# Kernel optimization log

Hardware: AMD Instinct MI355X
Metric: run time of the kernel (lower is better)

## Reference

```python
import jax, jax.numpy as jnp
import numpy as np

BLOCK = (4, 8, 8)   # (t, h, w)
NH, D, DA = 8, 512, 64
EPS = 1e-5


def _layernorm(x, g, b):
    m = jnp.mean(x, axis=-1, keepdims=True)
    xc = x - m
    v = jnp.mean(xc * xc, axis=-1, keepdims=True)
    return xc * jax.lax.rsqrt(v + EPS) * g + b


def setup_inputs() -> dict:
    key = jax.random.key(0)
    ks = jax.random.split(key, 10)
    B, T, H, W = 2, 8, 32, 32
    t, h, w = BLOCK
    s_qkv = (2.0 / (D + DA)) ** 0.5   # xavier_normal for (d, da) fan
    s_lin = (2.0 / (D + D)) ** 0.5
    return {
        "x": jax.random.normal(ks[0], (B, D, T, H, W), jnp.float32),
        "dt_bank": 0.02 * jax.random.normal(ks[1], (NH, 2 * t - 1), jnp.float32),
        "dh_bank": 0.02 * jax.random.normal(ks[2], (NH, 2 * h - 1), jnp.float32),
        "dw_bank": 0.02 * jax.random.normal(ks[3], (NH, 2 * w - 1), jnp.float32),
        "ln1_g": jnp.ones((D,), jnp.float32),
        "ln1_b": jnp.zeros((D,), jnp.float32),
        "w_q": s_qkv * jax.random.normal(ks[4], (NH, D, DA), jnp.float32),
        "w_k": s_qkv * jax.random.normal(ks[5], (NH, D, DA), jnp.float32),
        "w_v": s_qkv * jax.random.normal(ks[6], (NH, D, DA), jnp.float32),
        "w_proj": s_lin * jax.random.normal(ks[7], (D, NH * DA), jnp.float32),
        "ln2_g": jnp.ones((D,), jnp.float32),
        "ln2_b": jnp.zeros((D,), jnp.float32),
        "w1": s_lin * jax.random.normal(ks[8], (D, D), jnp.float32),
        "b1": jnp.zeros((D,), jnp.float32),
        "w2": s_lin * jax.random.normal(ks[9], (D, D), jnp.float32),
        "b2": jnp.zeros((D,), jnp.float32),
    }


def _axial_bias(dt_bank, dh_bank, dw_bank):
    t, h, w = BLOCK
    thw = t * h * w
    ar = jnp.arange(thw)
    tt = ar // (h * w)
    hh = (ar // w) % h
    ww = ar % w
    # relative offsets shifted to be non-negative (matches dt += abs(dt.min()))
    it = tt[:, None] - tt[None, :] + (t - 1)
    ih = hh[:, None] - hh[None, :] + (h - 1)
    iw = ww[:, None] - ww[None, :] + (w - 1)
    return dt_bank[:, it] + dh_bank[:, ih] + dw_bank[:, iw]  # (NH, thw, thw)


def reference(x, dt_bank, dh_bank, dw_bank, ln1_g, ln1_b, w_q, w_k, w_v,
              w_proj, ln2_g, ln2_b, w1, b1, w2, b2):
    B, C, T, H, W = x.shape
    t, h, w = BLOCK
    st, sh, sw = T // t, H // h, W // w
    thw = t * h * w
    nb = B * st * sh * sw

    # block split: (B,C,T,H,W) -> (nb, thw, C)
    xb = x.reshape(B, C, st, t, sh, h, sw, w).transpose(0, 2, 4, 6, 1, 3, 5, 7)
    xb = xb.reshape(nb, C, thw).transpose(0, 2, 1)

    Bb = _axial_bias(dt_bank, dh_bank, dw_bank)  # (NH, thw, thw)

    # --- multi-head attention with additive axial bias ---
    resid = xb
    xn = _layernorm(xb, ln1_g, ln1_b)
    q = jnp.einsum('bnd,hde->hbne', xn, w_q)
    k = jnp.einsum('bnd,hde->hbne', xn, w_k)
    v = jnp.einsum('bnd,hde->hbne', xn, w_v)
    scale = 1.0 / jnp.sqrt(jnp.asarray(DA, x.dtype))
    attn = jnp.einsum('hbne,hbme->hbnm', q, k) * scale + Bb[:, None]
    attn = jax.nn.softmax(attn, axis=-1)
    out = jnp.einsum('hbnm,hbme->hbne', attn, v)         # (NH, nb, thw, DA)
    out = out.transpose(1, 2, 0, 3).reshape(nb, thw, NH * DA)  # head-major concat
    out = out @ w_proj.T + resid

    # --- FFN with residual ---
    y = _layernorm(out, ln2_g, ln2_b)
    y = jax.nn.relu(y @ w1.T + b1) @ w2.T + b2
    out = y + out

    # un-block: (nb, thw, C) -> (B,C,T,H,W)
    out = out.transpose(0, 2, 1).reshape(B, st, sh, sw, C, t, h, w)
    out = out.transpose(0, 4, 1, 5, 2, 6, 3, 7).reshape(B, C, T, H, W)
    return out
```

## Files before the change

kernel.cpp:

```cpp
#include <hip/hip_runtime.h>
#include <hip/hip_bf16.h>
#include <stdint.h>

typedef __attribute__((ext_vector_type(4))) float f32x4;
typedef __attribute__((ext_vector_type(8))) short s16x8;
typedef __attribute__((ext_vector_type(4))) short s16x4;
typedef __attribute__((ext_vector_type(8))) __bf16 b16x8;

__device__ __forceinline__ f32x4 mfma16(s16x8 a, s16x8 b, f32x4 c) {
  return __builtin_amdgcn_mfma_f32_16x16x32_bf16(
      __builtin_bit_cast(b16x8, a), __builtin_bit_cast(b16x8, b), c, 0, 0, 0);
}

__device__ __forceinline__ void gl_lds16(const void* g, void* l) {
  __builtin_amdgcn_global_load_lds(
      (const __attribute__((address_space(1))) void*)g,
      (__attribute__((address_space(3))) void*)l, 16, 0, 0);
}

__device__ __forceinline__ unsigned short f2bf(float f) {
  union { float f; unsigned u; } v; v.f = f;
  unsigned u = v.u;
  return (unsigned short)((u + 0x7FFFu + ((u >> 16) & 1u)) >> 16);
}

__device__ __forceinline__ float bf2f(unsigned short u) {
  union { unsigned u; float f; } v; v.u = ((unsigned)u) << 16; return v.f;
}

__device__ __forceinline__ unsigned cvt_pk_bf16(float a, float b) {
  unsigned r;
  asm("v_cvt_pk_bf16_f32 %0, %1, %2" : "=v"(r) : "v"(a), "v"(b));
  return r;
}

#if __has_builtin(__builtin_amdgcn_exp2f)
#define EXP2F(x) __builtin_amdgcn_exp2f(x)
#else
#define EXP2F(x) exp2f(x)
#endif

__global__ __launch_bounds__(256) void k_gather_ln(
    const float* __restrict__ x, const float* __restrict__ g1, const float* __restrict__ b1,
    unsigned short* __restrict__ xb, unsigned short* __restrict__ xn,
    const float* __restrict__ wq, const float* __restrict__ wk, const float* __restrict__ wv,
    const float* __restrict__ wp, const float* __restrict__ w1, const float* __restrict__ w2,
    unsigned short* __restrict__ qkvT, unsigned short* __restrict__ wpT,
    unsigned short* __restrict__ w1T, unsigned short* __restrict__ w2T)
{
  if (blockIdx.x >= 1024) {
    int i = (blockIdx.x - 1024) * 256 + threadIdx.x;
    if (i < 786432) {
      int n = i >> 9, d = i & 511;
      const float* src = (n < 512) ? wq : (n < 1024 ? wk : wv);
      int nn = n & 511;
      int h = nn >> 6, e = nn & 63;
      qkvT[i] = f2bf(src[((size_t)h * 512 + d) * 64 + e]);
    } else {
      int j = i - 786432;
      int w = j >> 18;
      int o = j & 262143;
      const float* s = (w == 0) ? wp : (w == 1 ? w1 : w2);
      unsigned short* dst = (w == 0) ? wpT : (w == 1 ? w1T : w2T);
      dst[o] = f2bf(s[o]);
    }
    return;
  }
  __shared__ float lx[16][517];
  int gid = blockIdx.x;
  int h2 = gid & 1, hh = (gid >> 1) & 7, tt = (gid >> 4) & 3,
      shI = (gid >> 6) & 3, stI = (gid >> 8) & 1, bI = (gid >> 9) & 1;
  const float* xbase = x + (size_t)bI * 4194304 + (size_t)(stI * 4 + tt) * 1024
                       + (shI * 8 + hh) * 32 + h2 * 16;
  int t = threadIdx.x;
  for (int i = 0; i < 8; ++i) {
    int slot = i * 256 + t;
    int c = slot >> 2, w8 = slot & 3;
    const float4 v = *(const float4*)(xbase + (size_t)c * 8192 + w8 * 4);
    lx[w8 * 4 + 0][c] = v.x; lx[w8 * 4 + 1][c] = v.y;
    lx[w8 * 4 + 2][c] = v.z; lx[w8 * 4 + 3][c] = v.w;
  }
  __syncthreads();
  int lane = t & 63, wid = t >> 6;
  for (int q = 0; q < 4; ++q) {
    int widx = wid * 4 + q;
    float vv[8]; float s = 0.f, ss = 0.f;
    #pragma unroll
    for (int i = 0; i < 8; ++i) { float v = lx[widx][lane + i * 64]; vv[i] = v; s += v; ss += v * v; }
    #pragma unroll
    for (int d = 1; d < 64; d <<= 1) { s += __shfl_xor(s, d); ss += __shfl_xor(ss, d); }
    float mean = s * (1.f / 512.f);
    float var = ss * (1.f / 512.f) - mean * mean;
    float rs = rsqrtf(var + 1e-5f);
    int sw = h2 * 2 + (widx >> 3), ww = widx & 7;
    int blk = ((bI * 2 + stI) * 4 + shI) * 4 + sw;
    int n = tt * 64 + hh * 8 + ww;
    size_t base = ((size_t)blk * 256 + n) * 512;
    #pragma unroll
    for (int i = 0; i < 8; ++i) {
      int c = lane + i * 64;
      float v = vv[i];
      xb[base + c] = f2bf(v);
      xn[base + c] = f2bf((v - mean) * rs * g1[c] + b1[c]);
    }
  }
}

template<int EPI>
__global__ __launch_bounds__(256, 2) void k_gemm(
    const unsigned short* __restrict__ A, const unsigned short* __restrict__ Bt,
    int M, int N,
    unsigned short* __restrict__ Cbf, float* __restrict__ Cf,
    const float* __restrict__ bias,
    const unsigned short* __restrict__ addbf,
    unsigned short* __restrict__ vTout)
{
  constexpr int K = 512;
  __shared__ __align__(16) unsigned short a_lds[2][128 * 64];
  __shared__ __align__(16) unsigned short b_lds[2][128 * 64];
  int tid = threadIdx.x, lane = tid & 63, wid = tid >> 6;
  int lin = blockIdx.y * gridDim.x + blockIdx.x;
  int xcd = lin & 7, idx = lin >> 3;
  int bx = xcd * 16 + (idx & 15);
  int by = idx >> 4;
  int m0 = bx * 128, n0 = by * 128;
  int wm = (wid >> 1) * 64, wn = (wid & 1) * 64;
  int r15 = lane & 15, g = lane >> 4;

  const unsigned short* aptr[4];
  const unsigned short* bptr[4];
  int segoff[4];
  #pragma unroll
  for (int s = 0; s < 4; ++s) {
    int seg = wid * 4 + s;
    int slot = seg * 64 + lane;
    int m = slot >> 3, lc = (slot & 7) ^ (m & 7);
    aptr[s] = A + (size_t)(m0 + m) * K + lc * 8;
    bptr[s] = Bt + (size_t)(n0 + m) * K + lc * 8;
    segoff[s] = seg * 1024;
  }

  f32x4 acc[4][4] = {};

  #pragma unroll
  for (int s = 0; s < 4; ++s) {
    gl_lds16(aptr[s], (char*)a_lds[0] + segoff[s]);
    gl_lds16(bptr[s], (char*)b_lds[0] + segoff[s]);
  }

  #pragma unroll
  for (int it = 0; it < 8; ++it) {
    int cur = it & 1;
    if (it < 7) {
      int ksn = (it + 1) * 64;
      #pragma unroll
      for (int s = 0; s < 4; ++s) {
        gl_lds16(aptr[s] + ksn, (char*)a_lds[cur ^ 1] + segoff[s]);
        gl_lds16(bptr[s] + ksn, (char*)b_lds[cur ^ 1] + segoff[s]);
      }
      asm volatile("s_waitcnt vmcnt(8)" ::: "memory");
    } else {
      asm volatile("s_waitcnt vmcnt(0)" ::: "memory");
    }
    __builtin_amdgcn_s_barrier();
    __builtin_amdgcn_sched_barrier(0);
    const char* al = (const char*)a_lds[cur];
    const char* bl = (const char*)b_lds[cur];
    #pragma unroll
    for (int kk = 0; kk < 2; ++kk) {
      s16x8 af[4], bfr[4];
      #pragma unroll
      for (int f = 0; f < 4; ++f) {
        int mm = wm + f * 16 + r15;
        af[f] = *(const s16x8*)(al + mm * 128 + (((kk * 4 + g) ^ (mm & 7)) * 16));
        int nn = wn + f * 16 + r15;
        bfr[f] = *(const s16x8*)(bl + nn * 128 + (((kk * 4 + g) ^ (nn & 7)) * 16));
      }
      __builtin_amdgcn_s_setprio(1);
      #pragma unroll
      for (int fm = 0; fm < 4; ++fm)
        #pragma unroll
        for (int fn = 0; fn < 4; ++fn)
          acc[fm][fn] = mfma16(af[fm], bfr[fn], acc[fm][fn]);
      __builtin_amdgcn_s_setprio(0);
    }
    __builtin_amdgcn_s_barrier();
    __builtin_amdgcn_sched_barrier(0);
  }

  int g4 = g * 4;
  #pragma unroll
  for (int fm = 0; fm < 4; ++fm) {
    #pragma unroll
    for (int fn = 0; fn < 4; ++fn) {
      int col = n0 + wn + fn * 16 + r15;
      int row0 = m0 + wm + fm * 16 + g4;
      if (EPI == 0 && col >= 1024) {
        int h = (col - 1024) >> 6, e = col & 63;
        int blk = row0 >> 8, mtok = row0 & 255;
        s16x4 pk;
        #pragma unroll
        for (int r = 0; r < 4; ++r) pk[r] = (short)f2bf(acc[fm][fn][r]);
        *(s16x4*)(vTout + (((size_t)blk * 8 + h) * 64 + e) * 256 + mtok) = pk;
      } else {
        #pragma unroll
        for (int r = 0; r < 4; ++r) {
          int row = row0 + r;
          float v = acc[fm][fn][r];
          if (EPI == 0) {
            Cbf[(size_t)row * 1536 + col] = f2bf(v);
          } else if (EPI == 1) {
            Cbf[(size_t)row * 512 + col] = f2bf(v + bf2f(addbf[(size_t)row * 512 + col]));
          } else if (EPI == 2) {
            Cbf[(size_t)row * 512 + col] = f2bf(fmaxf(v + bias[col], 0.f));
          } else {
            Cf[(size_t)row * 512 + col] = v + bias[col] + bf2f(addbf[(size_t)row * 512 + col]);
          }
        }
      }
    }
  }
}

__global__ __launch_bounds__(256, 1) void k_attn(
    const unsigned short* __restrict__ qkv, const unsigned short* __restrict__ vT,
    const float* __restrict__ dtb, const float* __restrict__ dhb, const float* __restrict__ dwb,
    unsigned short* __restrict__ aout)
{
  __shared__ __align__(16) unsigned short k_lds[2][64 * 64];
  __shared__ __align__(16) unsigned short v_lds[2][64 * 64];
  __shared__ __align__(16) unsigned short p_lds[4][64 * 64];
  __shared__ float bt_s[8], bh_s[16], bw_s[16];

  const float L2E = 1.44269504f;
  const float SC = 0.125f * 1.44269504f;

  int tid = threadIdx.x, lane = tid & 63, wid = tid >> 6;
  int bk = blockIdx.x >> 3, h = blockIdx.x & 7;
  if (tid < 7) bt_s[tid] = dtb[h * 7 + tid] * L2E;
  else if (tid < 22) bh_s[tid - 7] = dhb[h * 15 + tid - 7] * L2E;
  else if (tid < 37) bw_s[tid - 22] = dwb[h * 15 + tid - 22] * L2E;

  int r15 = lane & 15, g = lane >> 4;
  int wq0 = wid * 64;
  size_t bkBase = (size_t)bk * 256;
  const unsigned short* kbase = qkv + 512 + h * 64;
  const unsigned short* vbase = vT + ((size_t)bk * 8 + h) * 64 * 256;

  s16x8 qf[4][2];
  #pragma unroll
  for (int fn = 0; fn < 4; ++fn)
    #pragma unroll
    for (int kk = 0; kk < 2; ++kk)
      qf[fn][kk] = *(const s16x8*)(qkv + (bkBase + wq0 + fn * 16 + r15) * 1536
                                   + h * 64 + kk * 32 + g * 8);

  float btoff[4], hb[7], wb[4];

  #pragma unroll
  for (int s = 0; s < 4; ++s) {
    int sg = wid * 4 + s;
    if (sg < 8) {
      int slot = sg * 64 + lane;
      int m = slot >> 3, lc = (slot & 7) ^ (m & 7);
      gl_lds16(kbase + (bkBase + m) * 1536 + lc * 8, (char*)(&k_lds[0][0]) + sg * 1024);
    } else {
      int sg2 = sg - 8;
      int slot = sg2 * 64 + lane;
      int e = slot >> 3, lc = (slot & 7) ^ (e & 7);
      gl_lds16(vbase + (size_t)e * 256 + lc * 8, (char*)(&v_lds[0][0]) + sg2 * 1024);
    }
  }
  __syncthreads();

  {
    int Dh = (r15 >> 3) - (g >> 1) + 7;
    int Wb = (r15 & 7) - 4 * (g & 1) + 7;
    #pragma unroll
    for (int mt = 0; mt < 4; ++mt) btoff[mt] = bt_s[wid + 3 - mt];
    #pragma unroll
    for (int d = 0; d < 7; ++d) hb[d] = bh_s[Dh + 2 * d - 6];
    #pragma unroll
    for (int r = 0; r < 4; ++r) wb[r] = bw_s[Wb - r];
  }

  f32x4 o[4][4] = {};
  float mrun[4] = {-1e30f, -1e30f, -1e30f, -1e30f};
  float lrun[4] = {0.f, 0.f, 0.f, 0.f};
  char* p_w = (char*)(&p_lds[wid][0]);

  #pragma unroll
  for (int mt = 0; mt < 4; ++mt) {
    int cur = mt & 1;
    if (mt < 3) {
      int m0n = (mt + 1) * 64;
      #pragma unroll
      for (int s = 0; s < 4; ++s) {
        int sg = wid * 4 + s;
        if (sg < 8) {
          int slot = sg * 64 + lane;
          int m = slot >> 3, lc = (slot & 7) ^ (m & 7);
          gl_lds16(kbase + (bkBase + m0n + m) * 1536 + lc * 8,
                   (char*)(&k_lds[cur ^ 1][0]) + sg * 1024);
        } else {
          int sg2 = sg - 8;
          int slot = sg2 * 64 + lane;
          int e = slot >> 3, lc = (slot & 7) ^ (e & 7);
          gl_lds16(vbase + (size_t)e * 256 + m0n + lc * 8,
                   (char*)(&v_lds[cur ^ 1][0]) + sg2 * 1024);
        }
      }
    }
    if (mt > 0) {
      if (mt < 3) asm volatile("s_waitcnt vmcnt(4)" ::: "memory");
      else        asm volatile("s_waitcnt vmcnt(0)" ::: "memory");
      __builtin_amdgcn_s_barrier();
      __builtin_amdgcn_sched_barrier(0);
    }
    const char* kl = (const char*)(&k_lds[cur][0]);
    const char* vl = (const char*)(&v_lds[cur][0]);

    f32x4 st[4][4] = {};
    #pragma unroll
    for (int kk = 0; kk < 2; ++kk) {
      s16x8 kf[4];
      #pragma unroll
      for (int fm = 0; fm < 4; ++fm) {
        int m = fm * 16 + r15;
        kf[fm] = *(const s16x8*)(kl + m * 128 + (((kk * 4 + g) ^ (m & 7)) * 16));
      }
      __builtin_amdgcn_s_setprio(1);
      #pragma unroll
      for (int fm = 0; fm < 4; ++fm)
        #pragma unroll
        for (int fn = 0; fn < 4; ++fn)
          st[fm][fn] = mfma16(kf[fm], qf[fn][kk], st[fm][fn]);
      __builtin_amdgcn_s_setprio(0);
    }

    #pragma unroll
    for (int fn = 0; fn < 4; ++fn) {
      float vals[16];
      float mx = -1e30f;
      #pragma unroll
      for (int fm = 0; fm < 4; ++fm) {
        float cc = btoff[mt] + hb[fn - fm + 3];
        #pragma unroll
        for (int r = 0; r < 4; ++r) {
          float v = fmaf(st[fm][fn][r], SC, cc) + wb[r];
          vals[fm * 4 + r] = v;
          mx = fmaxf(mx, v);
        }
      }
      mx = fmaxf(mx, __shfl_xor(mx, 16));
      mx = fmaxf(mx, __shfl_xor(mx, 32));
      if (!__all(mx <= mrun[fn] + 8.f)) {
        float mnew = fmaxf(mrun[fn], mx);
        float al = EXP2F(mrun[fn] - mnew);
        mrun[fn] = mnew;
        lrun[fn] *= al;
        #pragma unroll
        for (int fe = 0; fe < 4; ++fe)
          #pragma unroll
          for (int r = 0; r < 4; ++r)
            o[fe][fn][r] *= al;
      }
      float m_c = mrun[fn];
      float p[16]; float sum = 0.f;
      #pragma unroll
      for (int i = 0; i < 16; ++i) { p[i] = EXP2F(vals[i] - m_c); sum += p[i]; }
      sum += __shfl_xor(sum, 16);
      sum += __shfl_xor(sum, 32);
      lrun[fn] += sum;
      int nl = fn * 16 + r15;
      char* prow = p_w + nl * 128 + (g & 1) * 8;
      #pragma unroll
      for (int fm = 0; fm < 4; ++fm) {
        unsigned u0 = cvt_pk_bf16(p[fm * 4 + 0], p[fm * 4 + 1]);
        unsigned u1 = cvt_pk_bf16(p[fm * 4 + 2], p[fm * 4 + 3]);
        int lc = fm * 2 + (g >> 1);
        *(uint2*)(prow + ((lc ^ (nl & 7)) * 16)) = make_uint2(u0, u1);
      }
    }
    asm volatile("s_waitcnt lgkmcnt(0)" ::: "memory");
    __builtin_amdgcn_sched_barrier(0);

    #pragma unroll
    for (int mm = 0; mm < 2; ++mm) {
      s16x8 vf[4], pf[4];
      #pragma unroll
      for (int fe = 0; fe < 4; ++fe) {
        int e = fe * 16 + r15;
        vf[fe] = *(const s16x8*)(vl + e * 128 + (((mm * 4 + g) ^ (e & 7)) * 16));
      }
      #pragma unroll
      for (int fn = 0; fn < 4; ++fn) {
        int nl = fn * 16 + r15;
        pf[fn] = *(const s16x8*)(p_w + nl * 128 + (((mm * 4 + g) ^ (nl & 7)) * 16));
      }
      __builtin_amdgcn_s_setprio(1);
      #pragma unroll
      for (int fe = 0; fe < 4; ++fe)
        #pragma unroll
        for (int fn = 0; fn < 4; ++fn)
          o[fe][fn] = mfma16(vf[fe], pf[fn], o[fe][fn]);
      __builtin_amdgcn_s_setprio(0);
    }
    __builtin_amdgcn_s_barrier();
    __builtin_amdgcn_sched_barrier(0);
  }

  #pragma unroll
  for (int fn = 0; fn < 4; ++fn) {
    float inv = 1.f / lrun[fn];
    size_t rowb = (bkBase + wq0 + fn * 16 + r15) * 512 + h * 64;
    #pragma unroll
    for (int fe = 0; fe < 4; ++fe) {
      unsigned u0 = cvt_pk_bf16(o[fe][fn][0] * inv, o[fe][fn][1] * inv);
      unsigned u1 = cvt_pk_bf16(o[fe][fn][2] * inv, o[fe][fn][3] * inv);
      *(uint2*)(aout + rowb + fe * 16 + g * 4) = make_uint2(u0, u1);
    }
  }
}

__global__ __launch_bounds__(256) void k_ln2(
    const unsigned short* __restrict__ in, const float* __restrict__ g2, const float* __restrict__ b2,
    unsigned short* __restrict__ out)
{
  int token = blockIdx.x * 4 + (threadIdx.x >> 6);
  int lane = threadIdx.x & 63;
  s16x8 v8 = *(const s16x8*)(in + (size_t)token * 512 + lane * 8);
  float vv[8]; float s = 0.f, ss = 0.f;
  #pragma unroll
  for (int i = 0; i < 8; ++i) {
    float v = bf2f((unsigned short)v8[i]); vv[i] = v; s += v; ss += v * v;
  }
  #pragma unroll
  for (int d = 1; d < 64; d <<= 1) { s += __shfl_xor(s, d); ss += __shfl_xor(ss, d); }
  float mean = s * (1.f / 512.f);
  float var = ss * (1.f / 512.f) - mean * mean;
  float rs = rsqrtf(var + 1e-5f);
  const float4 gA = *(const float4*)(g2 + lane * 8);
  const float4 gB = *(const float4*)(g2 + lane * 8 + 4);
  const float4 bA = *(const float4*)(b2 + lane * 8);
  const float4 bB = *(const float4*)(b2 + lane * 8 + 4);
  float gv[8] = {gA.x, gA.y, gA.z, gA.w, gB.x, gB.y, gB.z, gB.w};
  float bv[8] = {bA.x, bA.y, bA.z, bA.w, bB.x, bB.y, bB.z, bB.w};
  s16x8 o8;
  #pragma unroll
  for (int i = 0; i < 8; ++i)
    o8[i] = (short)f2bf((vv[i] - mean) * rs * gv[i] + bv[i]);
  *(s16x8*)(out + (size_t)token * 512 + lane * 8) = o8;
}

__global__ __launch_bounds__(64) void k_scatter(
    const float* __restrict__ fin, float* __restrict__ out)
{
  __shared__ float lx[32][33];
  int gid = blockIdx.x;
  int cc = gid & 15;
  int sg = gid >> 4;
  int hh = sg & 7, tt = (sg >> 3) & 3, shI = (sg >> 5) & 3, stI = (sg >> 7) & 1, bI = (sg >> 8) & 1;
  int c0 = cc * 32;
  int l = threadIdx.x;
  #pragma unroll
  for (int i = 0; i < 4; ++i) {
    int slot = i * 64 + l;
    int tok = slot >> 3, c4 = slot & 7;
    int blk = ((bI * 2 + stI) * 4 + shI) * 4 + (tok >> 3);
    int n = tt * 64 + hh * 8 + (tok & 7);
    const float4 v = *(const float4*)(fin + ((size_t)blk * 256 + n) * 512 + c0 + c4 * 4);
    lx[tok][c4 * 4 + 0] = v.x; lx[tok][c4 * 4 + 1] = v.y;
    lx[tok][c4 * 4 + 2] = v.z; lx[tok][c4 * 4 + 3] = v.w;
  }
  __syncthreads();
  size_t obase = (size_t)bI * 4194304 + (size_t)(stI * 4 + tt) * 1024 + (shI * 8 + hh) * 32;
  #pragma unroll
  for (int i = 0; i < 4; ++i) {
    int crow = i * 8 + (l >> 3), w4 = l & 7;
    float4 v;
    v.x = lx[w4 * 4 + 0][crow]; v.y = lx[w4 * 4 + 1][crow];
    v.z = lx[w4 * 4 + 2][crow]; v.w = lx[w4 * 4 + 3][crow];
    *(float4*)(out + obase + (size_t)(c0 + crow) * 8192 + w4 * 4) = v;
  }
}

extern "C" void kernel_launch(void* const* d_in, const int* in_sizes, int n_in,
                              void* d_out, int out_size, void* d_ws, size_t ws_size,
                              hipStream_t stream)
{
  const float* x   = (const float*)d_in[0];
  const float* dtb = (const float*)d_in[1];
  const float* dhb = (const float*)d_in[2];
  const float* dwb = (const float*)d_in[3];
  const float* g1  = (const float*)d_in[4];
  const float* bb1 = (const float*)d_in[5];
  const float* wq  = (const float*)d_in[6];
  const float* wk  = (const float*)d_in[7];
  const float* wv  = (const float*)d_in[8];
  const float* wp  = (const float*)d_in[9];
  const float* g2  = (const float*)d_in[10];
  const float* bb2 = (const float*)d_in[11];
  const float* w1  = (const float*)d_in[12];
  const float* fb1 = (const float*)d_in[13];
  const float* w2  = (const float*)d_in[14];
  const float* fb2 = (const float*)d_in[15];

  char* ws = (char*)d_ws;
  unsigned short* xb   = (unsigned short*)(ws + 0);
  float*          finalb = (float*)(ws + 0);
  unsigned short* vT   = (unsigned short*)(ws + 33554432);
  unsigned short* out1b= (unsigned short*)(ws + 33554432);
  unsigned short* qkv  = (unsigned short*)(ws + 67108864);
  unsigned short* xn   = (unsigned short*)(ws + 117440512);
  unsigned short* qkvT = (unsigned short*)(ws + 134217728);
  unsigned short* wpT  = (unsigned short*)(ws + 135790592);
  unsigned short* w1T  = (unsigned short*)(ws + 136314880);
  unsigned short* w2T  = (unsigned short*)(ws + 136839168);

  unsigned short* attn_out = xn;
  unsigned short* yb = xn;
  unsigned short* h1 = qkv;
  float* outp = (float*)d_out;

  k_gather_ln<<<1024 + 6144, 256, 0, stream>>>(x, g1, bb1, xb, xn,
      wq, wk, wv, wp, w1, w2, qkvT, wpT, w1T, w2T);
  k_gemm<0><<<dim3(128, 12), 256, 0, stream>>>(xn, qkvT, 16384, 1536, qkv, nullptr, nullptr, nullptr, vT);
  k_attn<<<512, 256, 0, stream>>>(qkv, vT, dtb, dhb, dwb, attn_out);
  k_gemm<1><<<dim3(128, 4), 256, 0, stream>>>(attn_out, wpT, 16384, 512, out1b, nullptr, nullptr, xb, nullptr);
  k_ln2<<<4096, 256, 0, stream>>>(out1b, g2, bb2, yb);
  k_gemm<2><<<dim3(128, 4), 256, 0, stream>>>(yb, w1T, 16384, 512, h1, nullptr, fb1, nullptr, nullptr);
  k_gemm<3><<<dim3(128, 4), 256, 0, stream>>>(h1, w2T, 16384, 512, nullptr, finalb, fb2, out1b, nullptr);
  k_scatter<<<8192, 64, 0, stream>>>(finalb, outp);
}
```

Before: 156.9 us.

## Load GEMM B operand directly from global into registers, bypassing LDS

The B tile no longer goes through a double-buffered LDS staging area. Each wave now loads its own B fragments straight from global memory into a two-stage register buffer, one k-step ahead of use, and the vmcnt waits are adjusted to match. This halves the GEMM's LDS footprint and removes the LDS reads for B. In exchange, the two waves that share a column block both fetch the same B data, global accesses become row-strided 64-byte chunks, and register pressure rises by 16 vector fragments.

```diff
diff --git a/kernel.cpp b/kernel.cpp
--- a/kernel.cpp
+++ b/kernel.cpp
@@ -117,7 +117,6 @@
 {
   constexpr int K = 512;
   __shared__ __align__(16) unsigned short a_lds[2][128 * 64];
-  __shared__ __align__(16) unsigned short b_lds[2][128 * 64];
   int tid = threadIdx.x, lane = tid & 63, wid = tid >> 6;
   int lin = blockIdx.y * gridDim.x + blockIdx.x;
   int xcd = lin & 7, idx = lin >> 3;
@@ -128,7 +127,6 @@
   int r15 = lane & 15, g = lane >> 4;
 
   const unsigned short* aptr[4];
-  const unsigned short* bptr[4];
   int segoff[4];
   #pragma unroll
   for (int s = 0; s < 4; ++s) {
@@ -136,16 +134,19 @@
     int slot = seg * 64 + lane;
     int m = slot >> 3, lc = (slot & 7) ^ (m & 7);
     aptr[s] = A + (size_t)(m0 + m) * K + lc * 8;
-    bptr[s] = Bt + (size_t)(n0 + m) * K + lc * 8;
     segoff[s] = seg * 1024;
   }
+  const unsigned short* bbase = Bt + (size_t)(n0 + wn + r15) * K + g * 8;
 
   f32x4 acc[4][4] = {};
-
-  #pragma unroll
-  for (int s = 0; s < 4; ++s) {
-    gl_lds16(aptr[s], (char*)a_lds[0] + segoff[s]);
-    gl_lds16(bptr[s], (char*)b_lds[0] + segoff[s]);
+  s16x8 b[2][8];
+
+  #pragma unroll
+  for (int s = 0; s < 4; ++s) gl_lds16(aptr[s], (char*)a_lds[0] + segoff[s]);
+  #pragma unroll
+  for (int f = 0; f < 4; ++f) {
+    b[0][f * 2 + 0] = *(const s16x8*)(bbase + (size_t)(f * 16) * K);
+    b[0][f * 2 + 1] = *(const s16x8*)(bbase + (size_t)(f * 16) * K + 32);
   }
 
   #pragma unroll
@@ -154,34 +155,37 @@
     if (it < 7) {
       int ksn = (it + 1) * 64;
       #pragma unroll
-      for (int s = 0; s < 4; ++s) {
+      for (int s = 0; s < 4; ++s)
         gl_lds16(aptr[s] + ksn, (char*)a_lds[cur ^ 1] + segoff[s]);
-        gl_lds16(bptr[s] + ksn, (char*)b_lds[cur ^ 1] + segoff[s]);
-      }
-      asm volatile("s_waitcnt vmcnt(8)" ::: "memory");
+      asm volatile("s_waitcnt vmcnt(4)" ::: "memory");
     } else {
       asm volatile("s_waitcnt vmcnt(0)" ::: "memory");
     }
     __builtin_amdgcn_s_barrier();
     __builtin_amdgcn_sched_barrier(0);
+    if (it < 7) {
+      int ksn = (it + 1) * 64;
+      #pragma unroll
+      for (int f = 0; f < 4; ++f) {
+        b[cur ^ 1][f * 2 + 0] = *(const s16x8*)(bbase + (size_t)(f * 16) * K + ksn);
+        b[cur ^ 1][f * 2 + 1] = *(const s16x8*)(bbase + (size_t)(f * 16) * K + ksn + 32);
+      }
+    }
     const char* al = (const char*)a_lds[cur];
-    const char* bl = (const char*)b_lds[cur];
     #pragma unroll
     for (int kk = 0; kk < 2; ++kk) {
-      s16x8 af[4], bfr[4];
+      s16x8 af[4];
       #pragma unroll
       for (int f = 0; f < 4; ++f) {
         int mm = wm + f * 16 + r15;
         af[f] = *(const s16x8*)(al + mm * 128 + (((kk * 4 + g) ^ (mm & 7)) * 16));
-        int nn = wn + f * 16 + r15;
-        bfr[f] = *(const s16x8*)(bl + nn * 128 + (((kk * 4 + g) ^ (nn & 7)) * 16));
       }
       __builtin_amdgcn_s_setprio(1);
       #pragma unroll
       for (int fm = 0; fm < 4; ++fm)
         #pragma unroll
         for (int fn = 0; fn < 4; ++fn)
-          acc[fm][fn] = mfma16(af[fm], bfr[fn], acc[fm][fn]);
+          acc[fm][fn] = mfma16(af[fm], b[cur][fn * 2 + kk], acc[fm][fn]);
       __builtin_amdgcn_s_setprio(0);
     }
     __builtin_amdgcn_s_barrier();
```

Result: slower. 207.6 us (+32.3%).
